# Kernel tuning notes

Hardware: AMD Instinct MI355X
Metric: run time of the kernel (lower is better)

Reference implementation:

```python
import jax, jax.numpy as jnp
import numpy as np

MAX_W = 32  # static upper bound on window length (= max(ends - begins) in the torch code)


def setup_inputs() -> dict:
    key = jax.random.key(0)
    k1, k2, k3 = jax.random.split(key, 3)
    B, T, D, S = 8, 4096, 256, 1024
    features = jax.random.normal(k1, (B, T, D), dtype=jnp.float32)
    begins = jax.random.randint(k2, (B, S), 0, T - MAX_W)
    wins = jax.random.randint(k3, (B, S), 1, MAX_W + 1)
    ends = begins + wins
    return {"features": features, "begins": begins, "ends": ends}


def reference(features, begins, ends):
    # Pooler(mode='mean', dropout_p=0.0) ragged branch: for each span s in batch b,
    # mean of features[b, begins[b,s]:ends[b,s], :] (empty spans -> 0, matching
    # F.embedding_bag mean on an empty bag).
    B, T, D = features.shape
    begins = jnp.maximum(begins, 0)  # clamp_min(0) as in torch code
    ends = jnp.maximum(ends, 0)
    pos = begins[..., None] + jnp.arange(MAX_W)        # [B, S, W]
    valid = pos < ends[..., None]                      # [B, S, W]
    idx = jnp.clip(pos, 0, T - 1)
    gathered = jax.vmap(lambda f, i: f[i])(features, idx)   # [B, S, W, D]
    summed = jnp.sum(jnp.where(valid[..., None], gathered, 0.0), axis=2)  # [B, S, D]
    count = valid.sum(-1).astype(features.dtype)       # [B, S]
    return summed / jnp.maximum(count, 1.0)[..., None]
```

## Files before the change

kernel.cpp:

```cpp
#include <hip/hip_runtime.h>
#include <hip/hip_bf16.h>


#define B_DIM 8
#define T_DIM 4096
#define D_DIM 256
#define S_DIM 1024
#define MAX_W 32
#define NXCD 8

typedef float vfloat4 __attribute__((ext_vector_type(4)));

__global__ __launch_bounds__(256) void pooler_kernel(
    const float* __restrict__ features,
    const int*   __restrict__ begins,
    const int*   __restrict__ ends,
    float*       __restrict__ out)
{
    const int phys = blockIdx.x;
    const int lblk = (phys & (NXCD - 1)) * (2048 / NXCD) + (phys >> 3);

    const int span = lblk * 4 + (threadIdx.x >> 6);
    const int lane = threadIdx.x & 63;
    const int b = span >> 10;

    int begin = begins[span];
    int end   = ends[span];
    begin = begin > 0 ? begin : 0;
    end   = end   > 0 ? end   : 0;
    end   = end   < T_DIM ? end : T_DIM;
    int w = end - begin;
    w = w < MAX_W ? w : MAX_W;

    vfloat4* outp = reinterpret_cast<vfloat4*>(out + (size_t)span * D_DIM) + lane;

    if (w <= 0) {
        vfloat4 z = {0.f, 0.f, 0.f, 0.f};
        __builtin_nontemporal_store(z, outp);
        return;
    }

    const vfloat4* p = reinterpret_cast<const vfloat4*>(
        features + (size_t)b * T_DIM * D_DIM + (size_t)begin * D_DIM) + lane;

    vfloat4 acc = {0.f, 0.f, 0.f, 0.f};
    #pragma unroll 8
    for (int j = 0; j < w; ++j) {
        acc += p[(size_t)j * (D_DIM / 4)];
    }

    const float inv = 1.0f / (float)w;
    vfloat4 r = acc * inv;
    __builtin_nontemporal_store(r, outp);
}

extern "C" void kernel_launch(void* const* d_in, const int* in_sizes, int n_in,
                              void* d_out, int out_size, void* d_ws, size_t ws_size,
                              hipStream_t stream) {
    const float* features = (const float*)d_in[0];
    const int*   begins   = (const int*)d_in[1];
    const int*   ends     = (const int*)d_in[2];
    float*       out      = (float*)d_out;

    const int n_spans = B_DIM * S_DIM;
    const int blocks  = n_spans / 4;
    pooler_kernel<<<blocks, 256, 0, stream>>>(features, begins, ends, out);
}
```

Baseline: 14.39 us.

## Sort spans by begin position so adjacent blocks share cached feature rows

Adds a pre-pass kernel that bucket-sorts each batch's spans by begin position (16-row buckets) into a permutation held in workspace. The pooler then processes spans in that order, so neighbouring blocks read overlapping feature rows and hit in cache more often. This costs an extra kernel launch with a serial dependency, plus one extra indirect load per wavefront, and output writes become scattered. The sort only runs when the workspace is large enough.

```diff
diff --git a/kernel.cpp b/kernel.cpp
--- a/kernel.cpp
+++ b/kernel.cpp
@@ -11,18 +11,67 @@
 
 typedef float vfloat4 __attribute__((ext_vector_type(4)));
 
+__global__ __launch_bounds__(256) void sort_spans_kernel(
+    const int* __restrict__ begins,
+    int*       __restrict__ perm)
+{
+    const int b = blockIdx.x;
+    const int t = threadIdx.x;
+
+    __shared__ int hist[256];
+    __shared__ int scanbuf[256];
+
+    hist[t] = 0;
+    __syncthreads();
+
+    int key[4];
+    #pragma unroll
+    for (int k = 0; k < 4; ++k) {
+        const int s = t * 4 + k;
+        int bg = begins[b * S_DIM + s];
+        bg = bg > 0 ? bg : 0;
+        bg = bg < (T_DIM - 1) ? bg : (T_DIM - 1);
+        key[k] = bg >> 4;
+        atomicAdd(&hist[key[k]], 1);
+    }
+    __syncthreads();
+
+    int own = hist[t];
+    scanbuf[t] = own;
+    __syncthreads();
+    for (int off = 1; off < 256; off <<= 1) {
+        const int add = (t >= off) ? scanbuf[t - off] : 0;
+        __syncthreads();
+        scanbuf[t] += add;
+        __syncthreads();
+    }
+    hist[t] = scanbuf[t] - own;
+    __syncthreads();
+
+    #pragma unroll
+    for (int k = 0; k < 4; ++k) {
+        const int s = t * 4 + k;
+        const int pos = atomicAdd(&hist[key[k]], 1);
+        perm[b * S_DIM + pos] = s;
+    }
+}
+
 __global__ __launch_bounds__(256) void pooler_kernel(
     const float* __restrict__ features,
     const int*   __restrict__ begins,
     const int*   __restrict__ ends,
+    const int*   __restrict__ perm,
+    const int                 use_perm,
     float*       __restrict__ out)
 {
     const int phys = blockIdx.x;
     const int lblk = (phys & (NXCD - 1)) * (2048 / NXCD) + (phys >> 3);
 
-    const int span = lblk * 4 + (threadIdx.x >> 6);
+    const int slot = lblk * 4 + (threadIdx.x >> 6);
     const int lane = threadIdx.x & 63;
-    const int b = span >> 10;
+    const int b = slot >> 10;
+
+    const int span = use_perm ? (b * S_DIM + perm[slot]) : slot;
 
     int begin = begins[span];
     int end   = ends[span];
@@ -64,5 +113,13 @@
 
     const int n_spans = B_DIM * S_DIM;
     const int blocks  = n_spans / 4;
-    pooler_kernel<<<blocks, 256, 0, stream>>>(features, begins, ends, out);
+
+    int* perm = (int*)d_ws;
+    const int use_perm = (ws_size >= (size_t)n_spans * sizeof(int)) ? 1 : 0;
+
+    if (use_perm) {
+        sort_spans_kernel<<<B_DIM, 256, 0, stream>>>(begins, perm);
+    }
+    pooler_kernel<<<blocks, 256, 0, stream>>>(features, begins, ends,
+                                              perm, use_perm, out);
 }
```

Result: slower. 18.91 us (+31.4%).

## Compute span means via per-batch prefix sums and endpoint differences

Applied to the files above, without the earlier changes.

Adds a two-pass prefix-sum computation over the time axis (chunk sums in double, then per-chunk cumulative scan) written to workspace. Each span mean then needs only two row reads and a difference, replacing the per-span window loop. In exchange, the whole features tensor is read twice and a full-size prefix array is written, behind three kernel launches. Storing the prefix in float also risks cancellation error. The old direct kernel is kept as a fallback when the workspace is too small.

```diff
diff --git a/kernel.cpp b/kernel.cpp
--- a/kernel.cpp
+++ b/kernel.cpp
@@ -8,11 +8,52 @@
 #define S_DIM 1024
 #define MAX_W 32
 #define NXCD 8
+#define CHUNK 64
+#define NCHUNK (T_DIM / CHUNK)
 
 typedef float vfloat4 __attribute__((ext_vector_type(4)));
 
-__global__ __launch_bounds__(256) void pooler_kernel(
-    const float* __restrict__ features,
+__global__ __launch_bounds__(256) void chunk_sum_kernel(
+    const float* __restrict__ f,
+    double*      __restrict__ csum)
+{
+    const int phys = blockIdx.x;
+    const int b = phys & (NXCD - 1);
+    const int c = phys >> 3;
+    const int d = threadIdx.x;
+
+    const float* p = f + ((size_t)b * T_DIM + (size_t)c * CHUNK) * D_DIM + d;
+    double acc = 0.0;
+    #pragma unroll 16
+    for (int t = 0; t < CHUNK; ++t) acc += (double)p[(size_t)t * D_DIM];
+    csum[((size_t)b * NCHUNK + c) * D_DIM + d] = acc;
+}
+
+__global__ __launch_bounds__(256) void cumsum_kernel(
+    const float*  __restrict__ f,
+    const double* __restrict__ csum,
+    float*        __restrict__ P)
+{
+    const int phys = blockIdx.x;
+    const int b = phys & (NXCD - 1);
+    const int c = phys >> 3;
+    const int d = threadIdx.x;
+
+    double pref = 0.0;
+    const double* cs = csum + (size_t)b * NCHUNK * D_DIM + d;
+    for (int cc = 0; cc < c; ++cc) pref += cs[(size_t)cc * D_DIM];
+
+    const float* fp = f + ((size_t)b * T_DIM + (size_t)c * CHUNK) * D_DIM + d;
+    float*       Pp = P + ((size_t)b * T_DIM + (size_t)c * CHUNK) * D_DIM + d;
+    #pragma unroll 8
+    for (int t = 0; t < CHUNK; ++t) {
+        Pp[(size_t)t * D_DIM] = (float)pref;
+        pref += (double)fp[(size_t)t * D_DIM];
+    }
+}
+
+__global__ __launch_bounds__(256) void pool_diff_kernel(
+    const float* __restrict__ P,
     const int*   __restrict__ begins,
     const int*   __restrict__ ends,
     float*       __restrict__ out)
@@ -40,15 +81,49 @@
         return;
     }
 
+    const vfloat4* Pb = reinterpret_cast<const vfloat4*>(
+        P + ((size_t)b * T_DIM + begin) * D_DIM) + lane;
+    const vfloat4* Pe = reinterpret_cast<const vfloat4*>(
+        P + ((size_t)b * T_DIM + begin + w) * D_DIM) + lane;
+
+    const vfloat4 vb = *Pb;
+    const vfloat4 ve = *Pe;
+    const float inv = 1.0f / (float)w;
+    vfloat4 r = (ve - vb) * inv;
+    __builtin_nontemporal_store(r, outp);
+}
+
+__global__ __launch_bounds__(256) void pooler_direct_kernel(
+    const float* __restrict__ features,
+    const int*   __restrict__ begins,
+    const int*   __restrict__ ends,
+    float*       __restrict__ out)
+{
+    const int phys = blockIdx.x;
+    const int lblk = (phys & (NXCD - 1)) * (2048 / NXCD) + (phys >> 3);
+    const int span = lblk * 4 + (threadIdx.x >> 6);
+    const int lane = threadIdx.x & 63;
+    const int b = span >> 10;
+
+    int begin = begins[span];
+    int end   = ends[span];
+    begin = begin > 0 ? begin : 0;
+    end   = end   > 0 ? end   : 0;
+    end   = end   < T_DIM ? end : T_DIM;
+    int w = end - begin;
+    w = w < MAX_W ? w : MAX_W;
+
+    vfloat4* outp = reinterpret_cast<vfloat4*>(out + (size_t)span * D_DIM) + lane;
+    if (w <= 0) {
+        vfloat4 z = {0.f, 0.f, 0.f, 0.f};
+        __builtin_nontemporal_store(z, outp);
+        return;
+    }
     const vfloat4* p = reinterpret_cast<const vfloat4*>(
         features + (size_t)b * T_DIM * D_DIM + (size_t)begin * D_DIM) + lane;
-
     vfloat4 acc = {0.f, 0.f, 0.f, 0.f};
     #pragma unroll 8
-    for (int j = 0; j < w; ++j) {
-        acc += p[(size_t)j * (D_DIM / 4)];
-    }
-
+    for (int j = 0; j < w; ++j) acc += p[(size_t)j * (D_DIM / 4)];
     const float inv = 1.0f / (float)w;
     vfloat4 r = acc * inv;
     __builtin_nontemporal_store(r, outp);
@@ -62,7 +137,18 @@
     const int*   ends     = (const int*)d_in[2];
     float*       out      = (float*)d_out;
 
-    const int n_spans = B_DIM * S_DIM;
-    const int blocks  = n_spans / 4;
-    pooler_kernel<<<blocks, 256, 0, stream>>>(features, begins, ends, out);
+    const size_t P_bytes    = (size_t)B_DIM * T_DIM * D_DIM * sizeof(float);
+    const size_t csum_bytes = (size_t)B_DIM * NCHUNK * D_DIM * sizeof(double);
+
+    if (ws_size >= P_bytes + csum_bytes) {
+        float*  P    = (float*)d_ws;
+        double* csum = (double*)((char*)d_ws + P_bytes);
+
+        chunk_sum_kernel<<<B_DIM * NCHUNK, 256, 0, stream>>>(features, csum);
+        cumsum_kernel<<<B_DIM * NCHUNK, 256, 0, stream>>>(features, csum, P);
+        pool_diff_kernel<<<(B_DIM * S_DIM) / 4, 256, 0, stream>>>(P, begins, ends, out);
+    } else {
+        pooler_direct_kernel<<<(B_DIM * S_DIM) / 4, 256, 0, stream>>>(
+            features, begins, ends, out);
+    }
 }
```

New measurement: 36.73 us. +155.3%, slower.

## Stream window rows through LDS with double-buffered async global_load_lds

Applied to the files above, without the earlier changes.

Replaces direct vector global loads of each window row with asynchronous global-to-LDS copies in chunks of 8 rows, double-buffered per wave, with manual vmcnt waits before summing each chunk from LDS. The intent is to keep more memory requests in flight and overlap the fetch of the next chunk with accumulation of the current one. It adds 64KB of shared memory per block, which cuts occupancy, plus an extra LDS round trip. It also uses hand-written waitcnt asm without LDS barriers, relying on per-wave ordering for correctness.

```diff
diff --git a/kernel.cpp b/kernel.cpp
--- a/kernel.cpp
+++ b/kernel.cpp
@@ -10,6 +10,22 @@
 #define NXCD 8
 
 typedef float vfloat4 __attribute__((ext_vector_type(4)));
+typedef const __attribute__((address_space(1))) uint32_t* gptr_t;
+typedef __attribute__((address_space(3))) uint32_t* lptr_t;
+
+__device__ __forceinline__ void wait_vmcnt_n(int n) {
+    switch (n) {
+        case 0: asm volatile("s_waitcnt vmcnt(0)" ::: "memory"); break;
+        case 1: asm volatile("s_waitcnt vmcnt(1)" ::: "memory"); break;
+        case 2: asm volatile("s_waitcnt vmcnt(2)" ::: "memory"); break;
+        case 3: asm volatile("s_waitcnt vmcnt(3)" ::: "memory"); break;
+        case 4: asm volatile("s_waitcnt vmcnt(4)" ::: "memory"); break;
+        case 5: asm volatile("s_waitcnt vmcnt(5)" ::: "memory"); break;
+        case 6: asm volatile("s_waitcnt vmcnt(6)" ::: "memory"); break;
+        case 7: asm volatile("s_waitcnt vmcnt(7)" ::: "memory"); break;
+        default: asm volatile("s_waitcnt vmcnt(8)" ::: "memory"); break;
+    }
+}
 
 __global__ __launch_bounds__(256) void pooler_kernel(
     const float* __restrict__ features,
@@ -17,11 +33,14 @@
     const int*   __restrict__ ends,
     float*       __restrict__ out)
 {
+    __shared__ float lds[4][2][8][D_DIM];
+
     const int phys = blockIdx.x;
     const int lblk = (phys & (NXCD - 1)) * (2048 / NXCD) + (phys >> 3);
 
-    const int span = lblk * 4 + (threadIdx.x >> 6);
+    const int wid  = threadIdx.x >> 6;
     const int lane = threadIdx.x & 63;
+    const int span = lblk * 4 + wid;
     const int b = span >> 10;
 
     int begin = begins[span];
@@ -40,13 +59,42 @@
         return;
     }
 
-    const vfloat4* p = reinterpret_cast<const vfloat4*>(
-        features + (size_t)b * T_DIM * D_DIM + (size_t)begin * D_DIM) + lane;
+    const float* rowbase =
+        features + ((size_t)b * T_DIM + (size_t)begin) * D_DIM + lane * 4;
+
+    auto issue = [&](int k, int cnt) {
+        const float* g = rowbase + (size_t)(8 * k) * D_DIM;
+        float* lb = &lds[wid][k & 1][0][0];
+        for (int j = 0; j < cnt; ++j) {
+            __builtin_amdgcn_global_load_lds(
+                (gptr_t)(g + (size_t)j * D_DIM),
+                (lptr_t)(lb + j * D_DIM),
+                16, 0, 0);
+        }
+    };
 
     vfloat4 acc = {0.f, 0.f, 0.f, 0.f};
-    #pragma unroll 8
-    for (int j = 0; j < w; ++j) {
-        acc += p[(size_t)j * (D_DIM / 4)];
+    const int nb = (w + 7) >> 3;
+
+    int n0 = w > 8 ? 8 : w;
+    issue(0, n0);
+
+    for (int k = 0; k < nb; ++k) {
+        int nn = 0;
+        if (k + 1 < nb) {
+            nn = w - 8 * (k + 1);
+            nn = nn > 8 ? 8 : nn;
+            issue(k + 1, nn);
+        }
+        wait_vmcnt_n(nn);
+
+        const int cnt = (w - 8 * k) > 8 ? 8 : (w - 8 * k);
+        const vfloat4* lp =
+            reinterpret_cast<const vfloat4*>(&lds[wid][k & 1][0][0]) + lane;
+        #pragma unroll
+        for (int j = 0; j < 8; ++j) {
+            if (j < cnt) acc += lp[(size_t)j * (D_DIM / 4)];
+        }
     }
 
     const float inv = 1.0f / (float)w;
```

After: 23.02 us. 1.6x slower.
